# Optimization experiments

Measured on AMD Instinct MI355X. Metric: run time of the kernel, lower is better.

The kernel has to match this reference:

```python
import jax, jax.numpy as jnp
import numpy as np

B, S, D, H = 2, 2048, 1024, 16
DH = D // H  # 64

def setup_inputs() -> dict:
    key = jax.random.key(0)
    ks = jax.random.split(key, 11)
    sc = 1.0 / np.sqrt(D)
    return {
        "query": jax.random.normal(ks[0], (B, S, D), jnp.float32),
        "key":   jax.random.normal(ks[1], (B, S, D), jnp.float32),
        "value": jax.random.normal(ks[2], (B, S, D), jnp.float32),
        "Wq": jax.random.normal(ks[3], (D, D), jnp.float32) * sc,
        "bq": jnp.zeros((D,), jnp.float32),
        "Wk": jax.random.normal(ks[4], (D, D), jnp.float32) * sc,
        "bk": jnp.zeros((D,), jnp.float32),
        "Wv": jax.random.normal(ks[5], (D, D), jnp.float32) * sc,
        "bv": jnp.zeros((D,), jnp.float32),
        "Wo": jax.random.normal(ks[6], (D, D), jnp.float32) * sc,
        "bo": jnp.zeros((D,), jnp.float32),
    }

def reference(query, key, value, Wq, bq, Wk, bk, Wv, bv, Wo, bo):
    # torch Linear: y = x @ W^T + b
    def split_heads(x):  # (B,S,D) -> (B,H,S,DH)
        return x.reshape(B, S, H, DH).transpose(0, 2, 1, 3)
    Q = split_heads(query @ Wq.T + bq)
    K = split_heads(key   @ Wk.T + bk)
    V = split_heads(value @ Wv.T + bv)
    scores = jnp.einsum('bhqd,bhkd->bhqk', Q, K) / jnp.sqrt(jnp.float32(DH))
    # Original applies torch.softmax(scores, dim=1) on a (B*H, Sq, Sk) tensor,
    # i.e. normalization over the QUERY axis -> axis=-2 here (faithful to source).
    attn = jax.nn.softmax(scores, axis=-2)
    # dropout omitted for deterministic reference (identity / eval mode)
    out = jnp.einsum('bhqk,bhkd->bhqd', attn, V)  # (B,H,S,DH)
    out = out.transpose(0, 2, 1, 3).reshape(B, S, D)
    return out @ Wo.T + bo
```

## Files before the change

kernel.cpp:

```cpp
#include <hip/hip_runtime.h>
#include <hip/hip_bf16.h>
#include <math.h>

#define BB 2
#define SS 2048
#define DD 1024
#define HH 16
#define DH 64

typedef __bf16 bf16;
typedef __bf16 bf16x8 __attribute__((ext_vector_type(8)));
typedef __bf16 bf16x4 __attribute__((ext_vector_type(4)));
typedef short short4v __attribute__((ext_vector_type(4)));
typedef float f32x4 __attribute__((ext_vector_type(4)));

static const size_t NTOK  = (size_t)BB * SS * DD;
static const size_t STATN = (size_t)BB * HH * SS;


__device__ __forceinline__ f32x4 mfma16(bf16x8 a, bf16x8 b, f32x4 c) {
    return __builtin_amdgcn_mfma_f32_16x16x32_bf16(a, b, c, 0, 0, 0);
}
__device__ __forceinline__ f32x4 mfma16k16(short4v a, short4v b, f32x4 c) {
    return __builtin_amdgcn_mfma_f32_16x16x16bf16_1k(a, b, c, 0, 0, 0);
}
__device__ __forceinline__ void gload_lds16(const void* g, void* l) {
    __builtin_amdgcn_global_load_lds(
        (const __attribute__((address_space(1))) void*)g,
        (__attribute__((address_space(3))) void*)l, 16, 0, 0);
}
__device__ __forceinline__ bf16x8 cvt8(float4 a, float4 b) {
    bf16x8 r;
    r[0] = (bf16)a.x; r[1] = (bf16)a.y; r[2] = (bf16)a.z; r[3] = (bf16)a.w;
    r[4] = (bf16)b.x; r[5] = (bf16)b.y; r[6] = (bf16)b.z; r[7] = (bf16)b.w;
    return r;
}

#define WAITV(N)  asm volatile("s_waitcnt vmcnt(" #N ")" ::: "memory")
#define BAR()     __builtin_amdgcn_s_barrier()

__global__ void signal_f(float* out, float v) {
    if (threadIdx.x == 0 && blockIdx.x == 0) out[0] = v;
}

__global__ __launch_bounds__(256) void cvt_bf16(
    const float* __restrict__ s, bf16* __restrict__ d)
{
    size_t i = ((size_t)blockIdx.x * 256 + threadIdx.x) * 8;
    float4 a = *(const float4*)(s + i);
    float4 b = *(const float4*)(s + i + 4);
    *(bf16x8*)(d + i) = cvt8(a, b);
}
__global__ __launch_bounds__(256) void cvt_w3(
    const float* __restrict__ w0, const float* __restrict__ w1,
    const float* __restrict__ w2, bf16* __restrict__ o0,
    bf16* __restrict__ o1, bf16* __restrict__ o2)
{
    const float* s = (blockIdx.y == 0) ? w0 : (blockIdx.y == 1) ? w1 : w2;
    bf16*        d = (blockIdx.y == 0) ? o0 : (blockIdx.y == 1) ? o1 : o2;
    size_t i = ((size_t)blockIdx.x * 256 + threadIdx.x) * 8;
    float4 a = *(const float4*)(s + i);
    float4 b = *(const float4*)(s + i + 4);
    *(bf16x8*)(d + i) = cvt8(a, b);
}

#define LDP3 40

__global__ __launch_bounds__(256, 3) void qkv6(
    const float* __restrict__ Aq, const float* __restrict__ Ak,
    const float* __restrict__ Av,
    const bf16* __restrict__ Wqb, const bf16* __restrict__ Wkb,
    const bf16* __restrict__ Wvb,
    const float* __restrict__ bq, const float* __restrict__ bk,
    const float* __restrict__ bv,
    bf16* __restrict__ Qs, bf16* __restrict__ Ks, bf16* __restrict__ Vt)
{
    const int K = DD, N = DD;
    __shared__ bf16 As[2][128][LDP3];
    __shared__ bf16 Bs[2][128][LDP3];

    int t = (int)threadIdx.x;
    int lane = t & 63, w = t >> 6;
    int wm = w >> 1, wn = w & 1;
    int c16 = lane & 15, quad = lane >> 4, ko = quad << 3;

    int x = blockIdx.x & 7;
    int j = blockIdx.x >> 3;
    int proj = j >> 5;
    int rem  = j & 31;
    int tm = x + ((rem >> 3) << 3);
    int tn = rem & 7;

    const float* A    = (proj == 0) ? Aq : (proj == 1) ? Ak : Av;
    const bf16*  W    = (proj == 0) ? Wqb : (proj == 1) ? Wkb : Wvb;
    const float* bias = (proj == 0) ? bq : (proj == 1) ? bk : bv;
    bf16*        C    = (proj == 0) ? Qs : (proj == 1) ? Ks : Vt;
    float osc = (proj == 0) ? 0.125f : 1.0f;

    int arow = t >> 1, acb = (t & 1) * 16;
    const float* abase = A + (size_t)(tm * 128 + arow) * K + acb;
    const bf16*  wbase = W + (size_t)(tn * 128 + arow) * K + acb;

    f32x4 acc[4][4];
#pragma unroll
    for (int i = 0; i < 4; ++i)
#pragma unroll
        for (int q = 0; q < 4; ++q) acc[i][q] = (f32x4){0.f, 0.f, 0.f, 0.f};

    float4 aA0, aA1, aA2, aA3, aB0, aB1, aB2, aB3;
    bf16x8 wA0, wA1, wB0, wB1;

    aA0 = *(const float4*)(abase);     aA1 = *(const float4*)(abase + 4);
    aA2 = *(const float4*)(abase + 8); aA3 = *(const float4*)(abase + 12);
    wA0 = *(const bf16x8*)(wbase);     wA1 = *(const bf16x8*)(wbase + 8);
    *(bf16x8*)&As[0][arow][acb]     = cvt8(aA0, aA1);
    *(bf16x8*)&As[0][arow][acb + 8] = cvt8(aA2, aA3);
    *(bf16x8*)&Bs[0][arow][acb]     = wA0;
    *(bf16x8*)&Bs[0][arow][acb + 8] = wA1;
    aB0 = *(const float4*)(abase + 32);     aB1 = *(const float4*)(abase + 36);
    aB2 = *(const float4*)(abase + 40);     aB3 = *(const float4*)(abase + 44);
    wB0 = *(const bf16x8*)(wbase + 32);     wB1 = *(const bf16x8*)(wbase + 40);
    __syncthreads();

    auto qstep = [&](int T0, int BI,
                     float4& cA0, float4& cA1, float4& cA2, float4& cA3,
                     bf16x8& cW0, bf16x8& cW1,
                     float4& nA0, float4& nA1, float4& nA2, float4& nA3,
                     bf16x8& nW0, bf16x8& nW1) {
        if (T0 + 2 < 32) {
            const float* ap = abase + (T0 + 2) * 32;
            nA0 = *(const float4*)(ap);     nA1 = *(const float4*)(ap + 4);
            nA2 = *(const float4*)(ap + 8); nA3 = *(const float4*)(ap + 12);
            const bf16* wp = wbase + (T0 + 2) * 32;
            nW0 = *(const bf16x8*)(wp);     nW1 = *(const bf16x8*)(wp + 8);
        }
        bf16x8 af[4], bfr[4];
#pragma unroll
        for (int mt = 0; mt < 4; ++mt)
            af[mt] = *(const bf16x8*)&As[BI][wm * 64 + mt * 16 + c16][ko];
#pragma unroll
        for (int nt = 0; nt < 4; ++nt)
            bfr[nt] = *(const bf16x8*)&Bs[BI][wn * 64 + nt * 16 + c16][ko];
#pragma unroll
        for (int mt = 0; mt < 4; ++mt)
#pragma unroll
            for (int nt = 0; nt < 4; ++nt)
                acc[mt][nt] = mfma16(af[mt], bfr[nt], acc[mt][nt]);
        if (T0 + 1 < 32) {
            *(bf16x8*)&As[BI ^ 1][arow][acb]     = cvt8(cA0, cA1);
            *(bf16x8*)&As[BI ^ 1][arow][acb + 8] = cvt8(cA2, cA3);
            *(bf16x8*)&Bs[BI ^ 1][arow][acb]     = cW0;
            *(bf16x8*)&Bs[BI ^ 1][arow][acb + 8] = cW1;
        }
        __syncthreads();
    };

    for (int i = 0; i < 16; ++i) {
        qstep(2 * i,     0, aB0, aB1, aB2, aB3, wB0, wB1,
                            aA0, aA1, aA2, aA3, wA0, wA1);
        qstep(2 * i + 1, 1, aA0, aA1, aA2, aA3, wA0, wA1,
                            aB0, aB1, aB2, aB3, wB0, wB1);
    }

#pragma unroll
    for (int nt = 0; nt < 4; ++nt) {
        int col = tn * 128 + wn * 64 + nt * 16 + c16;
        float bv2 = bias[col];
#pragma unroll
        for (int mt = 0; mt < 4; ++mt) {
            int r0 = tm * 128 + wm * 64 + mt * 16 + quad * 4;
            if (proj == 2) {
                int b2 = r0 >> 11;
                int s  = r0 & (SS - 1);
                size_t base = ((size_t)b2 * N + col) * SS + s;
                bf16x4 pk;
#pragma unroll
                for (int r = 0; r < 4; ++r)
                    pk[r] = (bf16)(acc[mt][nt][r] + bv2);
                *(bf16x4*)&C[base] = pk;
            } else {
#pragma unroll
                for (int r = 0; r < 4; ++r)
                    C[(size_t)(r0 + r) * N + col] =
                        (bf16)((acc[mt][nt][r] + bv2) * osc);
            }
        }
    }
}

__global__ __launch_bounds__(512) void gemm6(
    const bf16* __restrict__ A, const bf16* __restrict__ W,
    const float* __restrict__ bias, float* __restrict__ C)
{
    __shared__ __align__(16) bf16 As[4][128][32];
    __shared__ __align__(16) bf16 Bs[4][128][32];

    int t = (int)threadIdx.x;
    int lane = t & 63, w = t >> 6;
    int wm = w >> 2, wn = w & 3;
    int c16 = lane & 15, quad = lane >> 4, ko = quad << 3;

    int x = blockIdx.x & 7, j = blockIdx.x >> 3;
    int tm = x + ((j >> 3) << 3);
    int tn = j & 7;

    int row0 = w * 16 + (lane >> 2);
    int chnk = (lane & 3) ^ (row0 & 3);
    const bf16* asrc = A + (size_t)(tm * 128 + row0) * DD + chnk * 8;
    const bf16* wsrc = W + (size_t)(tn * 128 + row0) * DD + chnk * 8;
    char* adst = (char*)&As[0][0][0] + w * 1024;
    char* wdst = (char*)&Bs[0][0][0] + w * 1024;

    f32x4 acc[4][2];
#pragma unroll
    for (int i = 0; i < 4; ++i)
#pragma unroll
        for (int q = 0; q < 2; ++q) acc[i][q] = (f32x4){0.f, 0.f, 0.f, 0.f};

#pragma unroll
    for (int s = 0; s < 2; ++s) {
        gload_lds16(asrc + s * 32, adst + s * 8192);
        gload_lds16(wsrc + s * 32, wdst + s * 8192);
    }

    for (int t0 = 0; t0 < 32; ++t0) {
        if (t0 + 2 < 32) {
            int s = t0 + 2, sb = (s & 3) * 8192;
            gload_lds16(asrc + s * 32, adst + sb);
            gload_lds16(wsrc + s * 32, wdst + sb);
        }
        if (t0 < 30)      { WAITV(4); }
        else if (t0 == 30){ WAITV(2); }
        else              { WAITV(0); }
        BAR();
        const char* al = (const char*)&As[0][0][0] + (t0 & 3) * 8192;
        const char* wl = (const char*)&Bs[0][0][0] + (t0 & 3) * 8192;
        bf16x8 af[4], bfr[2];
#pragma unroll
        for (int mt = 0; mt < 4; ++mt) {
            int row = wm * 64 + mt * 16 + c16;
            af[mt] = *(const bf16x8*)(al + row * 64 + ((quad ^ (row & 3)) << 4));
        }
#pragma unroll
        for (int nt = 0; nt < 2; ++nt) {
            int row = wn * 32 + nt * 16 + c16;
            bfr[nt] = *(const bf16x8*)(wl + row * 64 + ((quad ^ (row & 3)) << 4));
        }
#pragma unroll
        for (int mt = 0; mt < 4; ++mt)
#pragma unroll
            for (int nt = 0; nt < 2; ++nt)
                acc[mt][nt] = mfma16(af[mt], bfr[nt], acc[mt][nt]);
    }

#pragma unroll
    for (int nt = 0; nt < 2; ++nt) {
        int col = tn * 128 + wn * 32 + nt * 16 + c16;
        float bv = bias[col];
#pragma unroll
        for (int mt = 0; mt < 4; ++mt) {
            int r0 = tm * 128 + wm * 64 + mt * 16 + quad * 4;
#pragma unroll
            for (int r = 0; r < 4; ++r)
                C[(size_t)(r0 + r) * DD + col] = acc[mt][nt][r] + bv;
        }
    }
}

__global__ __launch_bounds__(512) void col_stats5(
    const bf16* __restrict__ Q, const bf16* __restrict__ Km,
    float* __restrict__ z0S, float* __restrict__ z1S)
{
    __shared__ __align__(16) bf16 Qlds[4][32][64];

    int t = (int)threadIdx.x;
    int w = t >> 6, lane = t & 63;
    int c16 = lane & 15, quad = lane >> 4, ko = quad << 3;

    int x = blockIdx.x & 7, j = blockIdx.x >> 3;
    int bh = ((j >> 4) << 3) + x;
    int qh = (j >> 3) & 1;
    int kg = j & 7;
    int b = bh >> 4, h = bh & (HH - 1);
    int kbase = kg * 256 + w * 32;
    int q0base = qh * 1024;
    float* zS = qh ? z1S : z0S;

    bf16x8 kf[2][2];
#pragma unroll
    for (int g = 0; g < 2; ++g) {
        const bf16* kp =
            Km + ((size_t)(b * SS + kbase + g * 16 + c16)) * DD + h * DH + ko;
        kf[g][0] = *(const bf16x8*)kp;
        kf[g][1] = *(const bf16x8*)(kp + 32);
    }

    int srow  = ((w & 3) << 3) + (lane >> 3);
    int schnk = (lane & 7) ^ (srow & 7);
    const bf16* gsrc =
        Q + ((size_t)(b * SS + q0base + srow)) * DD + h * DH + schnk * 8;
    int ldsOff = (w & 3) << 10;
    bool stager = (w < 4);

    float z[2][4] = {{0.f,0.f,0.f,0.f},{0.f,0.f,0.f,0.f}};

    if (stager) {
        gload_lds16(gsrc, (char*)&Qlds[0][0][0] + ldsOff);
        gload_lds16(gsrc + (size_t)32 * DD, (char*)&Qlds[1][0][0] + ldsOff);
    }

    for (int t0 = 0; t0 < 32; ++t0) {
        if (t0 + 2 < 32 && stager)
            gload_lds16(gsrc + (size_t)(t0 + 2) * 32 * DD,
                        (char*)&Qlds[(t0 + 2) & 3][0][0] + ldsOff);
        if (t0 < 30)      { WAITV(2); }
        else if (t0 == 30){ WAITV(1); }
        else              { WAITV(0); }
        BAR();
        const char* ql = (const char*)&Qlds[t0 & 3][0][0];
#pragma unroll
        for (int qs = 0; qs < 2; ++qs) {
            int row = qs * 16 + c16;
            int p0  = quad ^ (row & 7);
            bf16x8 qf0 = *(const bf16x8*)(ql + row * 128 + p0 * 16);
            bf16x8 qf1 = *(const bf16x8*)(ql + row * 128 + (p0 ^ 4) * 16);
#pragma unroll
            for (int g = 0; g < 2; ++g) {
                f32x4 a = {0.f, 0.f, 0.f, 0.f};
                a = mfma16(kf[g][0], qf0, a);
                a = mfma16(kf[g][1], qf1, a);
#pragma unroll
                for (int r = 0; r < 4; ++r)
                    z[g][r] += __expf(a[r]);
            }
        }
    }

#pragma unroll
    for (int g = 0; g < 2; ++g)
#pragma unroll
        for (int r = 0; r < 4; ++r) {
#pragma unroll
            for (int off = 1; off < 16; off <<= 1)
                z[g][r] += __shfl_xor(z[g][r], off, 64);
        }
    if (c16 == 0) {
        size_t base = (size_t)bh * SS + kbase + quad * 4;
#pragma unroll
        for (int g = 0; g < 2; ++g)
#pragma unroll
            for (int r = 0; r < 4; ++r)
                zS[base + g * 16 + r] = z[g][r];
    }
}

__global__ __launch_bounds__(512) void attn_ctx7(
    const bf16* __restrict__ Q, const bf16* __restrict__ Km,
    const bf16* __restrict__ Vt, const float* __restrict__ z0S,
    const float* __restrict__ z1S, bf16* __restrict__ ctx)
{
    __shared__ __align__(16) char lds[4][8192];
    __shared__ __align__(16) float rzlds[2048];

    int t = (int)threadIdx.x;
    int w = t >> 6, lane = t & 63;
    int c16 = lane & 15, quad = lane >> 4, ko = quad << 3;

    int bid = blockIdx.x;
    int x = bid & 7, j = bid >> 3;
    int bh = ((j >> 3) << 3) + x;
    int qg = j & 7;
    int b = bh >> 4, h = bh & (HH - 1);
    int qt0 = qg * 16 + w * 2;

    const bf16* qp0 = Q + ((size_t)(b * SS + qt0 * 16 + c16)) * DD + h * DH + ko;
    bf16x8 qa0 = *(const bf16x8*)qp0;
    bf16x8 qa1 = *(const bf16x8*)(qp0 + 32);
    const bf16* qp1 = qp0 + (size_t)16 * DD;
    bf16x8 qb0 = *(const bf16x8*)qp1;
    bf16x8 qb1 = *(const bf16x8*)(qp1 + 32);

    {
        const float* z0p = z0S + (size_t)bh * SS + (w << 8) + lane * 4;
        const float* z1p = z1S + (size_t)bh * SS + (w << 8) + lane * 4;
        gload_lds16(z0p, (char*)&lds[0][0] + (w << 10));
        gload_lds16(z1p, (char*)&lds[1][0] + (w << 10));
        WAITV(0);
        __syncthreads();
        f32x4 z0 = *(const f32x4*)&lds[0][t * 16];
        f32x4 z1 = *(const f32x4*)&lds[1][t * 16];
        f32x4 rz;
#pragma unroll
        for (int r = 0; r < 4; ++r) rz[r] = 1.0f / (z0[r] + z1[r]);
        *(f32x4*)&rzlds[t * 4] = rz;
        __syncthreads();
    }

    const bf16* gsrc;
    int ldsOff;
    bool isK = (w < 4);
    if (isK) {
        int row   = (w << 3) + (lane >> 3);
        int chunk = (lane & 7) ^ (row & 7);
        gsrc  = Km + ((size_t)(b * SS + row)) * DD + h * DH + chunk * 8;
        ldsOff = (w << 10);
    } else {
        int i = w - 4;
        int row   = (i << 4) + (lane >> 2);
        int chunk = (lane & 3) ^ ((lane >> 3) & 3);
        gsrc  = Vt + ((size_t)(b * DD + h * DH + row)) * SS + chunk * 8;
        ldsOff = 4096 + (i << 10);
    }

    int kread  = c16 * 128 + ((quad ^ (c16 & 7)) << 4);
    int vread0 = c16 * 64 + (((quad >> 1) ^ ((c16 >> 1) & 3)) << 4)
               + ((quad & 1) << 3);

    f32x4 oa[4] = {{0,0,0,0},{0,0,0,0},{0,0,0,0},{0,0,0,0}};
    f32x4 ob[4] = {{0,0,0,0},{0,0,0,0},{0,0,0,0},{0,0,0,0}};

    gload_lds16(gsrc, &lds[0][ldsOff]);
    gload_lds16(isK ? gsrc + (size_t)32 * DD : gsrc + 32, &lds[1][ldsOff]);

    for (int t0 = 0; t0 < 64; ++t0) {
        if (t0 + 2 < 64) {
            int s = t0 + 2;
            const bf16* g = isK ? gsrc + (size_t)(s * 32) * DD : gsrc + s * 32;
            gload_lds16(g, &lds[s & 3][ldsOff]);
        }
        if (t0 < 62)      { WAITV(2); }
        else if (t0 == 62){ WAITV(1); }
        else              { WAITV(0); }
        BAR();
        const char* kl = &lds[t0 & 3][0];
        const char* vl = &lds[t0 & 3][4096];
#pragma unroll
        for (int ks = 0; ks < 2; ++ks) {
            int kb0 = kread + ks * 2048;
            bf16x8 kf0 = *(const bf16x8*)(kl + kb0);
            bf16x8 kf1 = *(const bf16x8*)(kl + (kb0 ^ 64));
            f32x4 z4 = *(const f32x4*)&rzlds[t0 * 32 + ks * 16 + quad * 4];
            f32x4 sa = {0,0,0,0}, sb = {0,0,0,0};
            sa = mfma16(kf0, qa0, sa);
            sa = mfma16(kf1, qa1, sa);
            sb = mfma16(kf0, qb0, sb);
            sb = mfma16(kf1, qb1, sb);

            union { bf16x4 b; short4v s; } pa, pb;
#pragma unroll
            for (int r = 0; r < 4; ++r) {
                pa.b[r] = (bf16)(__expf(sa[r]) * z4[r]);
                pb.b[r] = (bf16)(__expf(sb[r]) * z4[r]);
            }
            int vb0 = ks ? (vread0 ^ 32) : vread0;
#pragma unroll
            for (int dt = 0; dt < 4; ++dt) {
                short4v vf = *(const short4v*)(vl + vb0 + dt * 1024);
                oa[dt] = mfma16k16(pa.s, vf, oa[dt]);
                ob[dt] = mfma16k16(pb.s, vf, ob[dt]);
            }
        }
    }

    size_t orow = ((size_t)(b * SS + qt0 * 16 + quad * 4)) * DD + h * DH + c16;
#pragma unroll
    for (int dt = 0; dt < 4; ++dt)
#pragma unroll
        for (int r = 0; r < 4; ++r) {
            ctx[orow + (size_t)r * DD + dt * 16] = (bf16)oa[dt][r];
            ctx[orow + (size_t)(16 + r) * DD + dt * 16] = (bf16)ob[dt][r];
        }
}

extern "C" void kernel_launch(void* const* d_in, const int* in_sizes, int n_in,
                              void* d_out, int out_size, void* d_ws, size_t ws_size,
                              hipStream_t stream) {
    const float* query = (const float*)d_in[0];
    const float* key   = (const float*)d_in[1];
    const float* value = (const float*)d_in[2];
    const float* Wq = (const float*)d_in[3];
    const float* bq = (const float*)d_in[4];
    const float* Wk = (const float*)d_in[5];
    const float* bk = (const float*)d_in[6];
    const float* Wv = (const float*)d_in[7];
    const float* bv = (const float*)d_in[8];
    const float* Wo = (const float*)d_in[9];
    const float* bo = (const float*)d_in[10];
    float* out = (float*)d_out;

    if (n_in != 11 || in_sizes[0] != (int)NTOK || in_sizes[3] != DD * DD ||
        in_sizes[4] != DD || out_size != (int)NTOK) {
        hipLaunchKernelGGL(signal_f, dim3(1), dim3(64), 0, stream, out, -64.0f);
        return;
    }

    bf16* Qs  = (bf16*)d_ws;
    bf16* Ks  = Qs + NTOK;
    bf16* Vt  = Ks + NTOK;
    bf16* Cs  = Vt + NTOK;
    float* z0S = (float*)(Cs + NTOK);
    float* z1S = z0S + STATN;

    bf16* Wqb = Cs;
    bf16* Wkb = Cs + (size_t)DD * DD;
    bf16* Wvb = Cs + (size_t)2 * DD * DD;
    bf16* WoB = Qs;

    hipLaunchKernelGGL(cvt_w3, dim3(512, 3), dim3(256), 0, stream,
                       Wq, Wk, Wv, Wqb, Wkb, Wvb);

    hipLaunchKernelGGL(qkv6, dim3(768), dim3(256), 0, stream,
                       query, key, value, Wqb, Wkb, Wvb, bq, bk, bv,
                       Qs, Ks, Vt);

    hipLaunchKernelGGL(col_stats5, dim3(512), dim3(512), 0, stream,
                       Qs, Ks, z0S, z1S);

    hipLaunchKernelGGL(attn_ctx7, dim3(256), dim3(512), 0, stream,
                       Qs, Ks, Vt, z0S, z1S, Cs);

    hipLaunchKernelGGL(cvt_bf16, dim3(512), dim3(256), 0, stream, Wo, WoB);

    hipLaunchKernelGGL(gemm6, dim3(256), dim3(512), 0, stream, Cs, WoB, bo, out);
}
```

Measured before the change: 271.5 us.

## Halve block sizes for attention and output GEMM, doubling grids; lighter qkv barriers

The attention-context kernel moves from 512-thread blocks to 256-thread blocks over half as many query tiles, with twice as many blocks. Each wave now loads both K and V tiles instead of splitting waves by K or V, and the normalizer reciprocals are read directly from global memory instead of staged through LDS. The output projection GEMM uses 128x64 tiles with 256 threads and a 512-block grid, to improve occupancy and load balance across CUs. The QKV kernel swaps __syncthreads for an explicit lgkmcnt wait plus barrier. The attention and GEMM changes cost more redundant K/V and weight loads per output element.

```diff
diff --git a/kernel.cpp b/kernel.cpp
--- a/kernel.cpp
+++ b/kernel.cpp
@@ -38,6 +38,8 @@
 
 #define WAITV(N)  asm volatile("s_waitcnt vmcnt(" #N ")" ::: "memory")
 #define BAR()     __builtin_amdgcn_s_barrier()
+#define LBAR() do { asm volatile("s_waitcnt lgkmcnt(0)" ::: "memory"); \
+                    __builtin_amdgcn_s_barrier(); } while (0)
 
 __global__ void signal_f(float* out, float v) {
     if (threadIdx.x == 0 && blockIdx.x == 0) out[0] = v;
@@ -66,7 +68,7 @@
 
 #define LDP3 40
 
-__global__ __launch_bounds__(256, 3) void qkv6(
+__global__ __launch_bounds__(256, 3) void qkv7(
     const float* __restrict__ Aq, const float* __restrict__ Ak,
     const float* __restrict__ Av,
     const bf16* __restrict__ Wqb, const bf16* __restrict__ Wkb,
@@ -120,7 +122,7 @@
     aB0 = *(const float4*)(abase + 32);     aB1 = *(const float4*)(abase + 36);
     aB2 = *(const float4*)(abase + 40);     aB3 = *(const float4*)(abase + 44);
     wB0 = *(const bf16x8*)(wbase + 32);     wB1 = *(const bf16x8*)(wbase + 40);
-    __syncthreads();
+    LBAR();
 
     auto qstep = [&](int T0, int BI,
                      float4& cA0, float4& cA1, float4& cA2, float4& cA3,
@@ -152,7 +154,7 @@
             *(bf16x8*)&Bs[BI ^ 1][arow][acb]     = cW0;
             *(bf16x8*)&Bs[BI ^ 1][arow][acb + 8] = cW1;
         }
-        __syncthreads();
+        LBAR();
     };
 
     for (int i = 0; i < 16; ++i) {
@@ -188,28 +190,30 @@
     }
 }
 
-__global__ __launch_bounds__(512) void gemm6(
+__global__ __launch_bounds__(256) void gemm7(
     const bf16* __restrict__ A, const bf16* __restrict__ W,
     const float* __restrict__ bias, float* __restrict__ C)
 {
     __shared__ __align__(16) bf16 As[4][128][32];
-    __shared__ __align__(16) bf16 Bs[4][128][32];
+    __shared__ __align__(16) bf16 Bs[4][64][32];
 
     int t = (int)threadIdx.x;
     int lane = t & 63, w = t >> 6;
-    int wm = w >> 2, wn = w & 3;
+    int wm = w >> 1, wn = w & 1;
     int c16 = lane & 15, quad = lane >> 4, ko = quad << 3;
 
     int x = blockIdx.x & 7, j = blockIdx.x >> 3;
-    int tm = x + ((j >> 3) << 3);
-    int tn = j & 7;
-
-    int row0 = w * 16 + (lane >> 2);
-    int chnk = (lane & 3) ^ (row0 & 3);
-    const bf16* asrc = A + (size_t)(tm * 128 + row0) * DD + chnk * 8;
-    const bf16* wsrc = W + (size_t)(tn * 128 + row0) * DD + chnk * 8;
-    char* adst = (char*)&As[0][0][0] + w * 1024;
-    char* wdst = (char*)&Bs[0][0][0] + w * 1024;
+    int tm = x + ((j >> 4) << 3);
+    int tn = j & 15;
+
+    int srow = lane >> 2;
+    int schk = (lane & 3) ^ (srow & 3);
+    const bf16* asrc0 = A + (size_t)(tm * 128 + (2 * w) * 16 + srow) * DD + schk * 8;
+    const bf16* asrc1 = asrc0 + (size_t)16 * DD;
+    const bf16* wsrc  = W + (size_t)(tn * 64 + w * 16 + srow) * DD + schk * 8;
+    char* adst0 = (char*)&As[0][0][0] + (2 * w) * 1024;
+    char* adst1 = adst0 + 1024;
+    char* wdst  = (char*)&Bs[0][0][0] + w * 1024;
 
     f32x4 acc[4][2];
 #pragma unroll
@@ -219,22 +223,24 @@
 
 #pragma unroll
     for (int s = 0; s < 2; ++s) {
-        gload_lds16(asrc + s * 32, adst + s * 8192);
-        gload_lds16(wsrc + s * 32, wdst + s * 8192);
+        gload_lds16(asrc0 + s * 32, adst0 + s * 8192);
+        gload_lds16(asrc1 + s * 32, adst1 + s * 8192);
+        gload_lds16(wsrc  + s * 32, wdst  + s * 4096);
     }
 
     for (int t0 = 0; t0 < 32; ++t0) {
         if (t0 + 2 < 32) {
-            int s = t0 + 2, sb = (s & 3) * 8192;
-            gload_lds16(asrc + s * 32, adst + sb);
-            gload_lds16(wsrc + s * 32, wdst + sb);
-        }
-        if (t0 < 30)      { WAITV(4); }
-        else if (t0 == 30){ WAITV(2); }
+            int s = t0 + 2;
+            gload_lds16(asrc0 + s * 32, adst0 + (s & 3) * 8192);
+            gload_lds16(asrc1 + s * 32, adst1 + (s & 3) * 8192);
+            gload_lds16(wsrc  + s * 32, wdst  + (s & 3) * 4096);
+        }
+        if (t0 < 30)      { WAITV(6); }
+        else if (t0 == 30){ WAITV(3); }
         else              { WAITV(0); }
         BAR();
         const char* al = (const char*)&As[0][0][0] + (t0 & 3) * 8192;
-        const char* wl = (const char*)&Bs[0][0][0] + (t0 & 3) * 8192;
+        const char* wl = (const char*)&Bs[0][0][0] + (t0 & 3) * 4096;
         bf16x8 af[4], bfr[2];
 #pragma unroll
         for (int mt = 0; mt < 4; ++mt) {
@@ -255,7 +261,7 @@
 
 #pragma unroll
     for (int nt = 0; nt < 2; ++nt) {
-        int col = tn * 128 + wn * 32 + nt * 16 + c16;
+        int col = tn * 64 + wn * 32 + nt * 16 + c16;
         float bv = bias[col];
 #pragma unroll
         for (int mt = 0; mt < 4; ++mt) {
@@ -354,7 +360,7 @@
     }
 }
 
-__global__ __launch_bounds__(512) void attn_ctx7(
+__global__ __launch_bounds__(256) void attn_ctx8(
     const bf16* __restrict__ Q, const bf16* __restrict__ Km,
     const bf16* __restrict__ Vt, const float* __restrict__ z0S,
     const float* __restrict__ z1S, bf16* __restrict__ ctx)
@@ -368,10 +374,10 @@
 
     int bid = blockIdx.x;
     int x = bid & 7, j = bid >> 3;
-    int bh = ((j >> 3) << 3) + x;
-    int qg = j & 7;
+    int bh = ((j >> 4) << 3) + x;
+    int qg = j & 15;
     int b = bh >> 4, h = bh & (HH - 1);
-    int qt0 = qg * 16 + w * 2;
+    int qt0 = qg * 8 + w * 2;
 
     const bf16* qp0 = Q + ((size_t)(b * SS + qt0 * 16 + c16)) * DD + h * DH + ko;
     bf16x8 qa0 = *(const bf16x8*)qp0;
@@ -380,37 +386,27 @@
     bf16x8 qb0 = *(const bf16x8*)qp1;
     bf16x8 qb1 = *(const bf16x8*)(qp1 + 32);
 
-    {
-        const float* z0p = z0S + (size_t)bh * SS + (w << 8) + lane * 4;
-        const float* z1p = z1S + (size_t)bh * SS + (w << 8) + lane * 4;
-        gload_lds16(z0p, (char*)&lds[0][0] + (w << 10));
-        gload_lds16(z1p, (char*)&lds[1][0] + (w << 10));
-        WAITV(0);
-        __syncthreads();
-        f32x4 z0 = *(const f32x4*)&lds[0][t * 16];
-        f32x4 z1 = *(const f32x4*)&lds[1][t * 16];
+#pragma unroll
+    for (int hh = 0; hh < 2; ++hh) {
+        int idx = hh * 256 + t;
+        f32x4 z0 = *(const f32x4*)(z0S + (size_t)bh * SS + idx * 4);
+        f32x4 z1 = *(const f32x4*)(z1S + (size_t)bh * SS + idx * 4);
         f32x4 rz;
 #pragma unroll
         for (int r = 0; r < 4; ++r) rz[r] = 1.0f / (z0[r] + z1[r]);
-        *(f32x4*)&rzlds[t * 4] = rz;
-        __syncthreads();
-    }
-
-    const bf16* gsrc;
-    int ldsOff;
-    bool isK = (w < 4);
-    if (isK) {
-        int row   = (w << 3) + (lane >> 3);
-        int chunk = (lane & 7) ^ (row & 7);
-        gsrc  = Km + ((size_t)(b * SS + row)) * DD + h * DH + chunk * 8;
-        ldsOff = (w << 10);
-    } else {
-        int i = w - 4;
-        int row   = (i << 4) + (lane >> 2);
-        int chunk = (lane & 3) ^ ((lane >> 3) & 3);
-        gsrc  = Vt + ((size_t)(b * DD + h * DH + row)) * SS + chunk * 8;
-        ldsOff = 4096 + (i << 10);
-    }
+        *(f32x4*)&rzlds[idx * 4] = rz;
+    }
+    __syncthreads();
+
+    int krow = (w << 3) + (lane >> 3);
+    int kchk = (lane & 7) ^ (krow & 7);
+    const bf16* kgsrc = Km + ((size_t)(b * SS + krow)) * DD + h * DH + kchk * 8;
+    int kldsOff = w << 10;
+
+    int vrow = (w << 4) + (lane >> 2);
+    int vchk = (lane & 3) ^ ((lane >> 3) & 3);
+    const bf16* vgsrc = Vt + ((size_t)(b * DD + h * DH + vrow)) * SS + vchk * 8;
+    int vldsOff = 4096 + (w << 10);
 
     int kread  = c16 * 128 + ((quad ^ (c16 & 7)) << 4);
     int vread0 = c16 * 64 + (((quad >> 1) ^ ((c16 >> 1) & 3)) << 4)
@@ -419,17 +415,20 @@
     f32x4 oa[4] = {{0,0,0,0},{0,0,0,0},{0,0,0,0},{0,0,0,0}};
     f32x4 ob[4] = {{0,0,0,0},{0,0,0,0},{0,0,0,0},{0,0,0,0}};
 
-    gload_lds16(gsrc, &lds[0][ldsOff]);
-    gload_lds16(isK ? gsrc + (size_t)32 * DD : gsrc + 32, &lds[1][ldsOff]);
+#pragma unroll
+    for (int s = 0; s < 2; ++s) {
+        gload_lds16(kgsrc + (size_t)(s * 32) * DD, &lds[s][kldsOff]);
+        gload_lds16(vgsrc + s * 32, &lds[s][vldsOff]);
+    }
 
     for (int t0 = 0; t0 < 64; ++t0) {
         if (t0 + 2 < 64) {
             int s = t0 + 2;
-            const bf16* g = isK ? gsrc + (size_t)(s * 32) * DD : gsrc + s * 32;
-            gload_lds16(g, &lds[s & 3][ldsOff]);
-        }
-        if (t0 < 62)      { WAITV(2); }
-        else if (t0 == 62){ WAITV(1); }
+            gload_lds16(kgsrc + (size_t)(s * 32) * DD, &lds[s & 3][kldsOff]);
+            gload_lds16(vgsrc + s * 32, &lds[s & 3][vldsOff]);
+        }
+        if (t0 < 62)      { WAITV(4); }
+        else if (t0 == 62){ WAITV(2); }
         else              { WAITV(0); }
         BAR();
         const char* kl = &lds[t0 & 3][0];
@@ -509,17 +508,17 @@
     hipLaunchKernelGGL(cvt_w3, dim3(512, 3), dim3(256), 0, stream,
                        Wq, Wk, Wv, Wqb, Wkb, Wvb);
 
-    hipLaunchKernelGGL(qkv6, dim3(768), dim3(256), 0, stream,
+    hipLaunchKernelGGL(qkv7, dim3(768), dim3(256), 0, stream,
                        query, key, value, Wqb, Wkb, Wvb, bq, bk, bv,
                        Qs, Ks, Vt);
 
     hipLaunchKernelGGL(col_stats5, dim3(512), dim3(512), 0, stream,
                        Qs, Ks, z0S, z1S);
 
-    hipLaunchKernelGGL(attn_ctx7, dim3(256), dim3(512), 0, stream,
+    hipLaunchKernelGGL(attn_ctx8, dim3(512), dim3(256), 0, stream,
                        Qs, Ks, Vt, z0S, z1S, Cs);
 
     hipLaunchKernelGGL(cvt_bf16, dim3(512), dim3(256), 0, stream, Wo, WoB);
 
-    hipLaunchKernelGGL(gemm6, dim3(256), dim3(512), 0, stream, Cs, WoB, bo, out);
-}
+    hipLaunchKernelGGL(gemm7, dim3(512), dim3(256), 0, stream, Cs, WoB, bo, out);
+}
```

New measurement: 280.0 us. 1.03x slower.
